# Optimization experiments

Hardware: AMD Instinct MI355X
Metric: run time of the kernel (lower is better)

The kernel has to match this reference:

```python
import jax, jax.numpy as jnp
import numpy as np

N, F_IN, H, C, E = 50000, 128, 4, 32, 800000
NEG_SLOPE = 0.2


def setup_inputs() -> dict:
    key = jax.random.key(0)
    ks = jax.random.split(key, 6)
    x = jax.random.normal(ks[0], (N, F_IN), dtype=jnp.float32)
    edge_index = jax.random.randint(ks[1], (2, E), 0, N, dtype=jnp.int64)
    scale = 1.0 / np.sqrt(F_IN)
    Wl = jax.random.normal(ks[2], (F_IN, H * C), dtype=jnp.float32) * scale
    Wr = jax.random.normal(ks[3], (F_IN, H * C), dtype=jnp.float32) * scale
    att = jax.random.normal(ks[4], (H, C), dtype=jnp.float32) * (1.0 / np.sqrt(C))
    bias = jax.random.normal(ks[5], (H * C,), dtype=jnp.float32) * 0.01
    return {"x": x, "edge_index": edge_index, "Wl": Wl, "Wr": Wr, "att": att, "bias": bias}


def reference(x, edge_index, Wl, Wr, att, bias):
    n = x.shape[0]
    # add self loops (add_self_loops=True, edge_dim=None)
    loop = jnp.arange(n, dtype=edge_index.dtype)
    ei = jnp.concatenate([edge_index, jnp.stack([loop, loop])], axis=1)
    src, dst = ei[0], ei[1]  # messages flow src -> dst; softmax over dst
    # share_weights=False: separate projections for source (l) and target (r)
    xl = (x @ Wl).reshape(n, H, C)
    xr = (x @ Wr).reshape(n, H, C)
    # GATv2 edge score: a . LeakyReLU(xl[src] + xr[dst])
    e = xl[src] + xr[dst]                      # [Et, H, C]
    e = jnp.where(e > 0, e, NEG_SLOPE * e)
    logits = jnp.einsum('ehc,hc->eh', e, att)  # [Et, H]
    # segment softmax over destination nodes (every node has a self loop)
    m = jax.ops.segment_max(logits, dst, num_segments=n)
    ex = jnp.exp(logits - m[dst])
    den = jax.ops.segment_sum(ex, dst, num_segments=n)
    alpha = ex / den[dst]                      # [Et, H]
    # weighted scatter-aggregate of source messages
    out = jax.ops.segment_sum(alpha[:, :, None] * xl[src], dst, num_segments=n)
    out = out.reshape(n, H * C) + bias         # concat=True heads, bias
    out = jax.nn.relu(out)                     # activation_func='relu'
    return out, alpha
```

## Files before the change

### kernel.cpp

```cpp
#include <hip/hip_runtime.h>
#include <hip/hip_bf16.h>
#include <hip/hip_fp16.h>

#define F_IN   128
#define HC     128
#define NH     4
#define NEG_SLOPE 0.2f
#define CAP2   48
#define NBUCK  196
#define EBLK   4096

typedef __attribute__((ext_vector_type(8))) short short8;
typedef __attribute__((ext_vector_type(4))) float f32x4;
typedef _Float16 h2 __attribute__((ext_vector_type(2)));

__device__ __forceinline__ unsigned short f2bf(float f) {
    union { float f; unsigned u; } c; c.f = f;
    unsigned u = c.u;
    u += 0x7FFFu + ((u >> 16) & 1u);
    return (unsigned short)(u >> 16);
}

__device__ __forceinline__ float fdot2f(h2 a, h2 b, float c) {
#if __has_builtin(__builtin_amdgcn_fdot2)
    return __builtin_amdgcn_fdot2(a, b, c, false);
#else
    return fmaf((float)a[0], (float)b[0], fmaf((float)a[1], (float)b[1], c));
#endif
}

union U4H { uint4 u; h2 h[4]; };

__global__ __launch_bounds__(256) void wpack_kernel(
    const float* __restrict__ Wl, const float* __restrict__ Wr,
    short* __restrict__ BlP, short* __restrict__ BrP)
{
    const int tid = blockIdx.x * 256 + threadIdx.x;
    const int mat = tid >> 11;
    const int r   = tid & 2047;
    const int f   = r >> 6;
    const int l   = r & 63;
    const int t   = f & 3;
    const int ct  = f >> 2;
    const int kb  = t * 32 + (l >> 4) * 8;
    const int c   = ct * 16 + (l & 15);
    const float* W = mat ? Wr : Wl;
    short*       P = mat ? BrP : BlP;
    short8 v;
    #pragma unroll
    for (int j = 0; j < 8; ++j)
        v[j] = (short)f2bf(W[(size_t)(kb + j) * HC + c]);
    *(short8*)&P[(size_t)(f * 64 + l) * 8] = v;
}

__global__ __launch_bounds__(1024) void proj_split_kernel(
    const float* __restrict__ x,
    const short* __restrict__ BlP,
    const short* __restrict__ BrP,
    unsigned short* __restrict__ xlb,
    unsigned short* __restrict__ xrb,
    const int* __restrict__ ei,
    int2* __restrict__ bucketRec,
    unsigned short* __restrict__ offT,
    int n, int E, int PB)
{
    __shared__ int  hist[256];
    __shared__ int  sc[256];
    __shared__ int2 stage[EBLK];
    const int t = threadIdx.x;

    if ((int)blockIdx.x >= PB) {
        const int sb = (int)blockIdx.x - PB;
        const int e0 = sb * EBLK;

        if (t < 256) hist[t] = 0;
        __syncthreads();

        int dsts[4], srcs[4], rk[4];
        #pragma unroll
        for (int k = 0; k < 4; ++k) {
            const int e = e0 + k * 1024 + t;
            dsts[k] = (e < E) ? ei[E + e] : -1;
            srcs[k] = (e < E) ? ei[e] : 0;
        }
        #pragma unroll
        for (int k = 0; k < 4; ++k)
            rk[k] = (dsts[k] >= 0) ? atomicAdd(&hist[dsts[k] >> 8], 1) : 0;
        __syncthreads();

        if (t < 256) sc[t] = hist[t];
        __syncthreads();
        for (int off = 1; off < 256; off <<= 1) {
            int v = 0, u = 0;
            if (t < 256) { v = sc[t]; u = (t >= off) ? sc[t - off] : 0; }
            __syncthreads();
            if (t < 256) sc[t] = v + u;
            __syncthreads();
        }
        if (t < NBUCK)
            offT[(size_t)sb * NBUCK + t] = (unsigned short)(sc[t] - hist[t]);

        #pragma unroll
        for (int k = 0; k < 4; ++k) {
            if (dsts[k] >= 0) {
                const int e   = e0 + k * 1024 + t;
                const int bkt = dsts[k] >> 8;
                const int base = sc[bkt] - hist[bkt];
                stage[base + rk[k]] =
                    make_int2(e | ((dsts[k] & 255) << 24), srcs[k]);
            }
        }
        __syncthreads();

        const int4* st4 = (const int4*)stage;
        int4* g4 = (int4*)(bucketRec + (size_t)sb * EBLK);
        g4[t]        = st4[t];
        g4[t + 1024] = st4[t + 1024];
        return;
    }

    const int w    = t >> 6;
    const int lane = t & 63;
    const int r0   = blockIdx.x * 256 + w * 16;
    if (r0 >= n) return;
    const int q    = lane >> 4;
    const int row  = r0 + (lane & 15);

    short8 af[4];
    {
        const float* xp = x + (size_t)row * F_IN + q * 8;
        #pragma unroll
        for (int s = 0; s < 4; ++s) {
            const float4 u0 = *(const float4*)(xp + s * 32);
            const float4 u1 = *(const float4*)(xp + s * 32 + 4);
            short8 a;
            a[0] = (short)f2bf(u0.x); a[1] = (short)f2bf(u0.y);
            a[2] = (short)f2bf(u0.z); a[3] = (short)f2bf(u0.w);
            a[4] = (short)f2bf(u1.x); a[5] = (short)f2bf(u1.y);
            a[6] = (short)f2bf(u1.z); a[7] = (short)f2bf(u1.w);
            af[s] = a;
        }
    }

    f32x4 accL[8], accR[8];
    const f32x4 zero = {0.f, 0.f, 0.f, 0.f};
    #pragma unroll
    for (int ct = 0; ct < 8; ++ct) { accL[ct] = zero; accR[ct] = zero; }

    #pragma unroll
    for (int s = 0; s < 4; ++s) {
        #pragma unroll
        for (int ct = 0; ct < 8; ++ct) {
            const short8 bl = *(const short8*)&BlP[(size_t)((ct * 4 + s) * 64 + lane) * 8];
            const short8 br = *(const short8*)&BrP[(size_t)((ct * 4 + s) * 64 + lane) * 8];
            accL[ct] = __builtin_amdgcn_mfma_f32_16x16x32_bf16(af[s], bl, accL[ct], 0, 0, 0);
            accR[ct] = __builtin_amdgcn_mfma_f32_16x16x32_bf16(af[s], br, accR[ct], 0, 0, 0);
        }
    }

    const int cb = lane & 15;
    const bool evenLane = (cb & 1) == 0;
    unsigned* xl_u = (unsigned*)xlb;
    unsigned* xr_u = (unsigned*)xrb;
    #pragma unroll
    for (int ct = 0; ct < 8; ++ct) {
        #pragma unroll
        for (int i = 0; i < 4; ++i) {
            const float l = accL[ct][i];
            const float r = accR[ct][i];
            const float sl = __shfl_xor(l, 1);
            const float sr = __shfl_xor(r, 1);
            const int rowo = r0 + q * 4 + i;
            const size_t cidx = (size_t)rowo * 64 + ct * 8 + (cb >> 1);
            union { _Float16 h[2]; unsigned u; } ph;
            if (evenLane) { ph.h[0] = (_Float16)l;  ph.h[1] = (_Float16)sl; xl_u[cidx] = ph.u; }
            else          { ph.h[0] = (_Float16)sr; ph.h[1] = (_Float16)r;  xr_u[cidx] = ph.u; }
        }
    }
}

__global__ __launch_bounds__(1024) void bucket_gather_kernel(
    const int2* __restrict__ bucketRec,
    const unsigned short* __restrict__ offT,
    int2* __restrict__ slot,
    int* __restrict__ cnt,
    int n, int E, int SB)
{
    __shared__ int sCnt[256];
    __shared__ int sOff[256];
    __shared__ int sI[256];
    __shared__ int cur[256];
    const int t = threadIdx.x;
    const int b = blockIdx.x;

    if (t < 256) {
        cur[t] = 0;
        int c = 0, o = 0;
        if (t < SB) {
            const int tot = min(EBLK, E - t * EBLK);
            o = offT[(size_t)t * NBUCK + b];
            const int o1 = (b < NBUCK - 1) ? (int)offT[(size_t)t * NBUCK + b + 1] : tot;
            c = o1 - o;
        }
        sCnt[t] = c; sOff[t] = o; sI[t] = c;
    }
    __syncthreads();
    for (int off = 1; off < 256; off <<= 1) {
        int v = 0, u = 0;
        if (t < 256) { v = sI[t]; u = (t >= off) ? sI[t - off] : 0; }
        __syncthreads();
        if (t < 256) sI[t] = v + u;
        __syncthreads();
    }
    const int cntB = sI[255];

    for (int i = t; i < cntB; i += 1024) {
        int lo = 0, hi = SB - 1;
        while (lo < hi) {
            const int mid = (lo + hi) >> 1;
            if (sI[mid] > i) hi = mid; else lo = mid + 1;
        }
        const int sb    = lo;
        const int local = i - (sI[sb] - sCnt[sb]);
        const int2 rec  = bucketRec[(size_t)sb * EBLK + sOff[sb] + local];
        const int dl  = (unsigned)rec.x >> 24;
        const int r   = atomicAdd(&cur[dl], 1);
        const int dst = (b << 8) + dl;
        if (r < CAP2)
            slot[(size_t)dst * CAP2 + r] = make_int2(rec.x & 0xFFFFFF, rec.y);
    }
    __syncthreads();
    if (t < 256) {
        const int dstT = (b << 8) + t;
        if (dstT < n) cnt[dstT] = cur[t];
    }
}

__global__ __launch_bounds__(256) void fused_agg_kernel(
    const int2* __restrict__ slot,
    const int* __restrict__ cnt,
    const unsigned short* __restrict__ xlb,
    const unsigned short* __restrict__ xrb,
    const float* __restrict__ att,
    const float* __restrict__ bias,
    float* __restrict__ alpha_out,
    float* __restrict__ out,
    int n, int E)
{
    __shared__ float lds_ex[4][256];
    const int w    = threadIdx.x >> 6;
    const int lane = threadIdx.x & 63;
    const int dst  = blockIdx.x * 4 + w;
    if (dst >= n) return;

    const int deg   = min(cnt[dst], CAP2);
    const int total = deg + 1;
    const int g     = lane >> 4;
    const int i     = lane & 15;
    const int h     = i >> 2;

    const char* xlB = (const char*)xlb;

    h2 xr2[4], at2[4];
    {
        U4H c; c.u = ((const uint4*)xrb)[(size_t)dst * 16 + i];
        xr2[0] = c.h[0]; xr2[1] = c.h[1]; xr2[2] = c.h[2]; xr2[3] = c.h[3];
        const float4 a01 = *(const float4*)&att[8 * i];
        const float4 a23 = *(const float4*)&att[8 * i + 4];
        at2[0] = h2{(_Float16)a01.x, (_Float16)a01.y};
        at2[1] = h2{(_Float16)a01.z, (_Float16)a01.w};
        at2[2] = h2{(_Float16)a23.x, (_Float16)a23.y};
        at2[3] = h2{(_Float16)a23.z, (_Float16)a23.w};
    }
    const h2 slope2 = {(_Float16)NEG_SLOPE, (_Float16)NEG_SLOPE};

    int eReg = E + dst, srcReg = dst;
    if (lane < deg) { const int2 es = slot[(size_t)dst * CAP2 + lane]; eReg = es.x; srcReg = es.y; }

    float* exrow = lds_ex[w];

    float dh = 0.f;
    float acc[8];
    #pragma unroll
    for (int k = 0; k < 8; ++k) acc[k] = 0.f;

    {
        const unsigned ib = (unsigned)i << 4;
        #define XLOAD(s) (*(const uint4*)(xlB + (((unsigned)(s) << 8) + ib)))

        const int s0 = __shfl(srcReg, g);
        uint4 u = XLOAD(s0);
        uint4 u1 = u, u2 = u, u3 = u;
        if (4 < total)  u1 = XLOAD(__shfl(srcReg, min(g + 4, 63)));
        if (8 < total)  u2 = XLOAD(__shfl(srcReg, min(g + 8, 63)));
        if (12 < total) u3 = XLOAD(__shfl(srcReg, min(g + 12, 63)));

        for (int j = 0; j < total; j += 4) {
            const int jj = j + g;
            uint4 u4 = u3;
            if (j + 16 < total) {
                const int sn = __shfl(srcReg, min(jj + 16, 63));
                u4 = XLOAD(sn);
            }

            U4H cu; cu.u = u;
            float p = 0.f;
            float vf[8];
            #pragma unroll
            for (int k = 0; k < 4; ++k) {
                const h2 v2 = cu.h[k];
                const h2 t2 = v2 + xr2[k];
                const h2 l2 = __builtin_elementwise_max(t2, t2 * slope2);
                p = fdot2f(l2, at2[k], p);
                vf[2 * k]     = (float)v2[0];
                vf[2 * k + 1] = (float)v2[1];
            }
            p += __shfl_xor(p, 1);
            p += __shfl_xor(p, 2);

            const float ex = (jj <= deg) ? __expf(p) : 0.f;
            dh += ex;
            #pragma unroll
            for (int k = 0; k < 8; ++k) acc[k] = fmaf(ex, vf[k], acc[k]);

            if ((lane & 3) == 0 && jj <= deg) exrow[jj * 4 + h] = ex;
            u = u1; u1 = u2; u2 = u3; u3 = u4;
        }
        #undef XLOAD
    }

    dh += __shfl_xor(dh, 16);
    dh += __shfl_xor(dh, 32);
    #pragma unroll
    for (int k = 0; k < 8; ++k) {
        acc[k] += __shfl_xor(acc[k], 16);
        acc[k] += __shfl_xor(acc[k], 32);
    }
    const float invh = 1.f / dh;
    const float id0 = 1.f / __shfl(dh, 0);
    const float id1 = 1.f / __shfl(dh, 4);
    const float id2 = 1.f / __shfl(dh, 8);
    const float id3 = 1.f / __shfl(dh, 12);

    __threadfence_block();

    if (lane < total) {
        const float4 e4 = *(const float4*)&exrow[lane * 4];
        const float4 a4 = make_float4(e4.x * id0, e4.y * id1, e4.z * id2, e4.w * id3);
        *(float4*)&alpha_out[(size_t)eReg * NH] = a4;
    }

    if (g == 0) {
        const float4 b01 = *(const float4*)&bias[8 * i];
        const float4 b23 = *(const float4*)&bias[8 * i + 4];
        float4 o01, o23;
        o01.x = fmaxf(fmaf(acc[0], invh, b01.x), 0.f);
        o01.y = fmaxf(fmaf(acc[1], invh, b01.y), 0.f);
        o01.z = fmaxf(fmaf(acc[2], invh, b01.z), 0.f);
        o01.w = fmaxf(fmaf(acc[3], invh, b01.w), 0.f);
        o23.x = fmaxf(fmaf(acc[4], invh, b23.x), 0.f);
        o23.y = fmaxf(fmaf(acc[5], invh, b23.y), 0.f);
        o23.z = fmaxf(fmaf(acc[6], invh, b23.z), 0.f);
        o23.w = fmaxf(fmaf(acc[7], invh, b23.w), 0.f);
        *(float4*)&out[(size_t)dst * HC + 8 * i]     = o01;
        *(float4*)&out[(size_t)dst * HC + 8 * i + 4] = o23;
    }
}

extern "C" void kernel_launch(void* const* d_in, const int* in_sizes, int n_in,
                              void* d_out, int out_size, void* d_ws, size_t ws_size,
                              hipStream_t stream)
{
    const float* x    = (const float*)d_in[0];
    const int*   ei   = (const int*)d_in[1];
    const float* Wl   = (const float*)d_in[2];
    const float* Wr   = (const float*)d_in[3];
    const float* att  = (const float*)d_in[4];
    const float* bias = (const float*)d_in[5];

    const int n  = in_sizes[0] / F_IN;
    const int E  = in_sizes[1] / 2;

    float* out   = (float*)d_out;
    float* alpha = (float*)d_out + (size_t)n * HC;

    const int SB = (E + EBLK - 1) / EBLK;
    const int PB = (n + 255) / 256;
    const int NB = (n + 255) >> 8;

    short*          BlP       = (short*)d_ws;
    short*          BrP       = BlP + 16384;
    unsigned short* xlb       = (unsigned short*)(BrP + 16384);
    unsigned short* xrb       = xlb + (size_t)n * HC;
    int2*           slot      = (int2*)(xrb + (size_t)n * HC);
    int*            cnt       = (int*)(slot + (size_t)n * CAP2);
    int2*           bucketRec = (int2*)(cnt + ((n + 3) & ~3));
    unsigned short* offT      = (unsigned short*)(bucketRec + (size_t)SB * EBLK);

    wpack_kernel<<<dim3(16), 256, 0, stream>>>(Wl, Wr, BlP, BrP);

    proj_split_kernel<<<dim3(PB + SB), 1024, 0, stream>>>(
        x, BlP, BrP, xlb, xrb, ei, bucketRec, offT, n, E, PB);

    bucket_gather_kernel<<<dim3(NB), 1024, 0, stream>>>(
        bucketRec, offT, slot, cnt, n, E, SB);

    fused_agg_kernel<<<dim3((n + 3) / 4), 256, 0, stream>>>(
        slot, cnt, xlb, xrb, att, bias, alpha, out, n, E);
}
```

Measured before the change: 161.0 us.

## Regroup stages into two launches: weight-pack+edge split, then projection+bucket gather

Merges the weight packing kernel with the edge bucketing (split) stage, and merges the dense projection with the bucket gather stage, cutting four launches down to three. Each merged kernel dispatches independent work by block index, so the projection now runs concurrently with the gather instead of with the split. The intent is to remove one launch and dependency boundary and to overlap independent stages better. The cost is that the split stage now runs on its own before the projection and no longer hides behind it, and the merged kernels carry the larger shared-memory footprint of their combined roles.

```diff
diff --git a/kernel.cpp b/kernel.cpp
--- a/kernel.cpp
+++ b/kernel.cpp
@@ -31,91 +31,149 @@
 
 union U4H { uint4 u; h2 h[4]; };
 
-__global__ __launch_bounds__(256) void wpack_kernel(
+__global__ __launch_bounds__(1024) void wpack_split_kernel(
     const float* __restrict__ Wl, const float* __restrict__ Wr,
-    short* __restrict__ BlP, short* __restrict__ BrP)
+    short* __restrict__ BlP, short* __restrict__ BrP,
+    const int* __restrict__ ei,
+    int2* __restrict__ bucketRec,
+    unsigned short* __restrict__ offT,
+    int E)
 {
-    const int tid = blockIdx.x * 256 + threadIdx.x;
-    const int mat = tid >> 11;
-    const int r   = tid & 2047;
-    const int f   = r >> 6;
-    const int l   = r & 63;
-    const int t   = f & 3;
-    const int ct  = f >> 2;
-    const int kb  = t * 32 + (l >> 4) * 8;
-    const int c   = ct * 16 + (l & 15);
-    const float* W = mat ? Wr : Wl;
-    short*       P = mat ? BrP : BlP;
-    short8 v;
-    #pragma unroll
-    for (int j = 0; j < 8; ++j)
-        v[j] = (short)f2bf(W[(size_t)(kb + j) * HC + c]);
-    *(short8*)&P[(size_t)(f * 64 + l) * 8] = v;
-}
-
-__global__ __launch_bounds__(1024) void proj_split_kernel(
+    __shared__ int  hist[256];
+    __shared__ int  sc[256];
+    __shared__ int2 stage[EBLK];
+    const int t = threadIdx.x;
+
+    if ((int)blockIdx.x < 4) {
+        const int tid = (int)blockIdx.x * 1024 + t;
+        const int mat = tid >> 11;
+        const int r   = tid & 2047;
+        const int f   = r >> 6;
+        const int l   = r & 63;
+        const int tt  = f & 3;
+        const int ct  = f >> 2;
+        const int kb  = tt * 32 + (l >> 4) * 8;
+        const int c   = ct * 16 + (l & 15);
+        const float* W = mat ? Wr : Wl;
+        short*       P = mat ? BrP : BlP;
+        short8 v;
+        #pragma unroll
+        for (int j = 0; j < 8; ++j)
+            v[j] = (short)f2bf(W[(size_t)(kb + j) * HC + c]);
+        *(short8*)&P[(size_t)(f * 64 + l) * 8] = v;
+        return;
+    }
+
+    const int sb = (int)blockIdx.x - 4;
+    const int e0 = sb * EBLK;
+
+    if (t < 256) hist[t] = 0;
+    __syncthreads();
+
+    int dsts[4], srcs[4], rk[4];
+    #pragma unroll
+    for (int k = 0; k < 4; ++k) {
+        const int e = e0 + k * 1024 + t;
+        dsts[k] = (e < E) ? ei[E + e] : -1;
+        srcs[k] = (e < E) ? ei[e] : 0;
+    }
+    #pragma unroll
+    for (int k = 0; k < 4; ++k)
+        rk[k] = (dsts[k] >= 0) ? atomicAdd(&hist[dsts[k] >> 8], 1) : 0;
+    __syncthreads();
+
+    if (t < 256) sc[t] = hist[t];
+    __syncthreads();
+    for (int off = 1; off < 256; off <<= 1) {
+        int v = 0, u = 0;
+        if (t < 256) { v = sc[t]; u = (t >= off) ? sc[t - off] : 0; }
+        __syncthreads();
+        if (t < 256) sc[t] = v + u;
+        __syncthreads();
+    }
+    if (t < NBUCK)
+        offT[(size_t)sb * NBUCK + t] = (unsigned short)(sc[t] - hist[t]);
+
+    #pragma unroll
+    for (int k = 0; k < 4; ++k) {
+        if (dsts[k] >= 0) {
+            const int e    = e0 + k * 1024 + t;
+            const int bkt  = dsts[k] >> 8;
+            const int base = sc[bkt] - hist[bkt];
+            stage[base + rk[k]] =
+                make_int2(e | ((dsts[k] & 255) << 24), srcs[k]);
+        }
+    }
+    __syncthreads();
+
+    const int4* st4 = (const int4*)stage;
+    int4* g4 = (int4*)(bucketRec + (size_t)sb * EBLK);
+    g4[t]        = st4[t];
+    g4[t + 1024] = st4[t + 1024];
+}
+
+__global__ __launch_bounds__(1024) void proj_gather_kernel(
     const float* __restrict__ x,
     const short* __restrict__ BlP,
     const short* __restrict__ BrP,
     unsigned short* __restrict__ xlb,
     unsigned short* __restrict__ xrb,
-    const int* __restrict__ ei,
-    int2* __restrict__ bucketRec,
-    unsigned short* __restrict__ offT,
-    int n, int E, int PB)
+    const int2* __restrict__ bucketRec,
+    const unsigned short* __restrict__ offT,
+    int2* __restrict__ slot,
+    int* __restrict__ cnt,
+    int n, int E, int PB, int SB)
 {
-    __shared__ int  hist[256];
-    __shared__ int  sc[256];
-    __shared__ int2 stage[EBLK];
+    __shared__ int sCnt[256];
+    __shared__ int sOff[256];
+    __shared__ int sI[256];
+    __shared__ int cur[256];
     const int t = threadIdx.x;
 
     if ((int)blockIdx.x >= PB) {
-        const int sb = (int)blockIdx.x - PB;
-        const int e0 = sb * EBLK;
-
-        if (t < 256) hist[t] = 0;
-        __syncthreads();
-
-        int dsts[4], srcs[4], rk[4];
-        #pragma unroll
-        for (int k = 0; k < 4; ++k) {
-            const int e = e0 + k * 1024 + t;
-            dsts[k] = (e < E) ? ei[E + e] : -1;
-            srcs[k] = (e < E) ? ei[e] : 0;
-        }
-        #pragma unroll
-        for (int k = 0; k < 4; ++k)
-            rk[k] = (dsts[k] >= 0) ? atomicAdd(&hist[dsts[k] >> 8], 1) : 0;
-        __syncthreads();
-
-        if (t < 256) sc[t] = hist[t];
+        const int b = (int)blockIdx.x - PB;
+
+        if (t < 256) {
+            cur[t] = 0;
+            int c = 0, o = 0;
+            if (t < SB) {
+                const int tot = min(EBLK, E - t * EBLK);
+                o = offT[(size_t)t * NBUCK + b];
+                const int o1 = (b < NBUCK - 1) ? (int)offT[(size_t)t * NBUCK + b + 1] : tot;
+                c = o1 - o;
+            }
+            sCnt[t] = c; sOff[t] = o; sI[t] = c;
+        }
         __syncthreads();
         for (int off = 1; off < 256; off <<= 1) {
             int v = 0, u = 0;
-            if (t < 256) { v = sc[t]; u = (t >= off) ? sc[t - off] : 0; }
+            if (t < 256) { v = sI[t]; u = (t >= off) ? sI[t - off] : 0; }
             __syncthreads();
-            if (t < 256) sc[t] = v + u;
+            if (t < 256) sI[t] = v + u;
             __syncthreads();
         }
-        if (t < NBUCK)
-            offT[(size_t)sb * NBUCK + t] = (unsigned short)(sc[t] - hist[t]);
-
-        #pragma unroll
-        for (int k = 0; k < 4; ++k) {
-            if (dsts[k] >= 0) {
-                const int e   = e0 + k * 1024 + t;
-                const int bkt = dsts[k] >> 8;
-                const int base = sc[bkt] - hist[bkt];
-                stage[base + rk[k]] =
-                    make_int2(e | ((dsts[k] & 255) << 24), srcs[k]);
+        const int cntB = sI[255];
+
+        for (int i = t; i < cntB; i += 1024) {
+            int lo = 0, hi = SB - 1;
+            while (lo < hi) {
+                const int mid = (lo + hi) >> 1;
+                if (sI[mid] > i) hi = mid; else lo = mid + 1;
             }
+            const int sb    = lo;
+            const int local = i - (sI[sb] - sCnt[sb]);
+            const int2 rec  = bucketRec[(size_t)sb * EBLK + sOff[sb] + local];
+            const int dl  = (unsigned)rec.x >> 24;
+            const int r   = atomicAdd(&cur[dl], 1);
+            const int dst = (b << 8) + dl;
+            if (r < CAP2)
+                slot[(size_t)dst * CAP2 + r] = make_int2(rec.x & 0xFFFFFF, rec.y);
         }
         __syncthreads();
-
-        const int4* st4 = (const int4*)stage;
-        int4* g4 = (int4*)(bucketRec + (size_t)sb * EBLK);
-        g4[t]        = st4[t];
-        g4[t + 1024] = st4[t + 1024];
+        if (t < 256) {
+            const int dstT = (b << 8) + t;
+            if (dstT < n) cnt[dstT] = cur[t];
+        }
         return;
     }
 
@@ -176,63 +234,6 @@
             if (evenLane) { ph.h[0] = (_Float16)l;  ph.h[1] = (_Float16)sl; xl_u[cidx] = ph.u; }
             else          { ph.h[0] = (_Float16)sr; ph.h[1] = (_Float16)r;  xr_u[cidx] = ph.u; }
         }
-    }
-}
-
-__global__ __launch_bounds__(1024) void bucket_gather_kernel(
-    const int2* __restrict__ bucketRec,
-    const unsigned short* __restrict__ offT,
-    int2* __restrict__ slot,
-    int* __restrict__ cnt,
-    int n, int E, int SB)
-{
-    __shared__ int sCnt[256];
-    __shared__ int sOff[256];
-    __shared__ int sI[256];
-    __shared__ int cur[256];
-    const int t = threadIdx.x;
-    const int b = blockIdx.x;
-
-    if (t < 256) {
-        cur[t] = 0;
-        int c = 0, o = 0;
-        if (t < SB) {
-            const int tot = min(EBLK, E - t * EBLK);
-            o = offT[(size_t)t * NBUCK + b];
-            const int o1 = (b < NBUCK - 1) ? (int)offT[(size_t)t * NBUCK + b + 1] : tot;
-            c = o1 - o;
-        }
-        sCnt[t] = c; sOff[t] = o; sI[t] = c;
-    }
-    __syncthreads();
-    for (int off = 1; off < 256; off <<= 1) {
-        int v = 0, u = 0;
-        if (t < 256) { v = sI[t]; u = (t >= off) ? sI[t - off] : 0; }
-        __syncthreads();
-        if (t < 256) sI[t] = v + u;
-        __syncthreads();
-    }
-    const int cntB = sI[255];
-
-    for (int i = t; i < cntB; i += 1024) {
-        int lo = 0, hi = SB - 1;
-        while (lo < hi) {
-            const int mid = (lo + hi) >> 1;
-            if (sI[mid] > i) hi = mid; else lo = mid + 1;
-        }
-        const int sb    = lo;
-        const int local = i - (sI[sb] - sCnt[sb]);
-        const int2 rec  = bucketRec[(size_t)sb * EBLK + sOff[sb] + local];
-        const int dl  = (unsigned)rec.x >> 24;
-        const int r   = atomicAdd(&cur[dl], 1);
-        const int dst = (b << 8) + dl;
-        if (r < CAP2)
-            slot[(size_t)dst * CAP2 + r] = make_int2(rec.x & 0xFFFFFF, rec.y);
-    }
-    __syncthreads();
-    if (t < 256) {
-        const int dstT = (b << 8) + t;
-        if (dstT < n) cnt[dstT] = cur[t];
     }
 }
 
@@ -397,13 +398,11 @@
     int2*           bucketRec = (int2*)(cnt + ((n + 3) & ~3));
     unsigned short* offT      = (unsigned short*)(bucketRec + (size_t)SB * EBLK);
 
-    wpack_kernel<<<dim3(16), 256, 0, stream>>>(Wl, Wr, BlP, BrP);
-
-    proj_split_kernel<<<dim3(PB + SB), 1024, 0, stream>>>(
-        x, BlP, BrP, xlb, xrb, ei, bucketRec, offT, n, E, PB);
-
-    bucket_gather_kernel<<<dim3(NB), 1024, 0, stream>>>(
-        bucketRec, offT, slot, cnt, n, E, SB);
+    wpack_split_kernel<<<dim3(4 + SB), 1024, 0, stream>>>(
+        Wl, Wr, BlP, BrP, ei, bucketRec, offT, E);
+
+    proj_gather_kernel<<<dim3(PB + NB), 1024, 0, stream>>>(
+        x, BlP, BrP, xlb, xrb, bucketRec, offT, slot, cnt, n, E, PB, SB);
 
     fused_agg_kernel<<<dim3((n + 3) / 4), 256, 0, stream>>>(
         slot, cnt, xlb, xrb, att, bias, alpha, out, n, E);
```

After: 157.0 us, median of 2. 2.5% less time.
